# Kernel optimization log

Measured on AMD Instinct MI355X. Metric: run time of the kernel, lower is better.

Reference implementation:

```python
import jax, jax.numpy as jnp
import numpy as np

B, N, C, H = 16, 207, 64, 64

def setup_inputs() -> dict:
    key = jax.random.key(0)
    k1, k2, k3, k4, k5 = jax.random.split(key, 5)
    return {
        "x": jax.random.normal(k1, (B, N, C), dtype=jnp.float32),
        "state": jax.random.normal(k2, (B, N, 1, H), dtype=jnp.float32),
        "Wx": jax.random.normal(k3, (B, N, C, 3 * H), dtype=jnp.float32) * 0.1,
        "Wh": jax.random.normal(k4, (B, N, H, 3 * H), dtype=jnp.float32) * 0.1,
        "b": jax.random.normal(k5, (B, N, 1, 3 * H), dtype=jnp.float32) * 0.1,
    }

def reference(x, state, Wx, Wh, b):
    # x: [B,N,C] -> [B,N,1,C]; state (h): [B,N,1,H]
    if x.ndim == 3:
        x = x[..., None, :]
    h = state
    dim_hidden = Wh.shape[-2]
    # One fused batched matmul for x @ Wx, then split into r/z/c parts.
    xW = jnp.matmul(x, Wx)  # [B,N,1,3H]
    xr, xz, xc = jnp.split(xW, 3, axis=-1)
    Wrh, Wzh, Wch = jnp.split(Wh, 3, axis=-1)
    br, bz, bc = jnp.split(b, 3, axis=-1)
    r = jax.nn.sigmoid(xr + jnp.matmul(h, Wrh) + br)
    z = jax.nn.sigmoid(xz + jnp.matmul(h, Wzh) + bz)
    # Note torch precedence: r * h @ Wch == (r * h) @ Wch
    hc = jnp.tanh(xc + jnp.matmul(r * h, Wch) + bc)
    h_new = (1.0 - z) * h + z * hc  # [B,N,1,H]
    return h_new
```

## Files before the change

### kernel.cpp

```cpp
#include <hip/hip_runtime.h>
#include <math.h>


#define GC 64
#define GH 64
#define J3 192
#define WPP (GC * J3)

__global__ __launch_bounds__(192) void gru_cell_v2(
    const float* __restrict__ x,
    const float* __restrict__ state,
    const float* __restrict__ Wx,
    const float* __restrict__ Wh,
    const float* __restrict__ b,
    float* __restrict__ out)
{
    const int pos = blockIdx.x;
    const int t = threadIdx.x;
    const int jg = t % 48;
    const int rp = t / 48;

    __shared__ float x_s[GC];
    __shared__ float h_s[GH];
    __shared__ float wch_s[GC * GH];
    __shared__ float part[4][J3 + 4];
    __shared__ float rh_s[GH];
    __shared__ float z_s[GH];

    if (t < GC)           x_s[t]      = x[(size_t)pos * GC + t];
    else if (t < GC + GH) h_s[t - GC] = state[(size_t)pos * GH + (t - GC)];
    __syncthreads();

    const float4* __restrict__ Wx4 = (const float4*)(Wx + (size_t)pos * WPP);
    const float4* __restrict__ Wh4 = (const float4*)(Wh + (size_t)pos * WPP);

    float4 acc = {0.f, 0.f, 0.f, 0.f};
    const bool gate = (jg < 32);
    const int wchcol = 4 * (jg - 32);

    #pragma unroll 4
    for (int i = 0; i < 16; ++i) {
        const int c = 4 * i + rp;
        float4 wx4 = Wx4[i * J3 + t];
        float4 wh4 = Wh4[i * J3 + t];
        const float xs = x_s[c];
        acc.x += xs * wx4.x; acc.y += xs * wx4.y;
        acc.z += xs * wx4.z; acc.w += xs * wx4.w;
        if (gate) {
            const float hs = h_s[c];
            acc.x += hs * wh4.x; acc.y += hs * wh4.y;
            acc.z += hs * wh4.z; acc.w += hs * wh4.w;
        } else {
            *((float4*)&wch_s[c * GH + wchcol]) = wh4;
        }
    }

    *((float4*)&part[rp][4 * jg]) = acc;
    __syncthreads();

    float v = part[0][t] + part[1][t] + part[2][t] + part[3][t]
            + b[(size_t)pos * J3 + t];
    const float tc = v;
    if (t < GH) {
        float r = 1.f / (1.f + expf(-v));
        rh_s[t] = r * h_s[t];
    } else if (t < 2 * GH) {
        z_s[t - GH] = 1.f / (1.f + expf(-v));
    }
    __syncthreads();

    if (t >= 2 * GH) {
        const int jc = t - 2 * GH;
        float s = 0.f;
        #pragma unroll 8
        for (int k = 0; k < GH; ++k) s += rh_s[k] * wch_s[k * GH + jc];
        const float hc = tanhf(tc + s);
        const float z = z_s[jc];
        out[(size_t)pos * GH + jc] = (1.f - z) * h_s[jc] + z * hc;
    }
}

extern "C" void kernel_launch(void* const* d_in, const int* in_sizes, int n_in,
                              void* d_out, int out_size, void* d_ws, size_t ws_size,
                              hipStream_t stream) {
    const float* x     = (const float*)d_in[0];
    const float* state = (const float*)d_in[1];
    const float* Wx    = (const float*)d_in[2];
    const float* Wh    = (const float*)d_in[3];
    const float* b     = (const float*)d_in[4];
    float* out = (float*)d_out;

    const int npos = in_sizes[0] / GC;

    gru_cell_v2<<<npos, 192, 0, stream>>>(x, state, Wx, Wh, b, out);
}
```

Measured before the change: 337.5 us.

## Split GRU cell into r-gate phase then z/candidate phase with 256 threads

Restructures the per-position kernel into two phases. The first computes only the r gate from the first 64 columns of Wx/Wh. The second computes the z gate and the candidate, folding r*h into the Wh matmul so Wch no longer needs to be staged in shared memory. Block size grows to 256 with a 16- or 8-way row split, shared memory use drops, and the launch bound asks for more resident blocks. The cost is extra syncthreads, and the second half of the weights is read only after the r gate is done, which serializes part of the memory streaming.

```diff
diff --git a/kernel.cpp b/kernel.cpp
--- a/kernel.cpp
+++ b/kernel.cpp
@@ -7,7 +7,7 @@
 #define J3 192
 #define WPP (GC * J3)
 
-__global__ __launch_bounds__(192) void gru_cell_v2(
+__global__ __launch_bounds__(256, 8) void gru_cell_v3(
     const float* __restrict__ x,
     const float* __restrict__ state,
     const float* __restrict__ Wx,
@@ -17,66 +17,84 @@
 {
     const int pos = blockIdx.x;
     const int t = threadIdx.x;
-    const int jg = t % 48;
-    const int rp = t / 48;
 
     __shared__ float x_s[GC];
-    __shared__ float h_s[GH];
-    __shared__ float wch_s[GC * GH];
-    __shared__ float part[4][J3 + 4];
-    __shared__ float rh_s[GH];
+    __shared__ float mult_s[2 * GH];
+    __shared__ float part[1024];
     __shared__ float z_s[GH];
 
-    if (t < GC)           x_s[t]      = x[(size_t)pos * GC + t];
-    else if (t < GC + GH) h_s[t - GC] = state[(size_t)pos * GH + (t - GC)];
+    if (t < GC)           x_s[t]          = x[(size_t)pos * GC + t];
+    else if (t < GC + GH) mult_s[t - GC]  = state[(size_t)pos * GH + (t - GC)];
     __syncthreads();
 
     const float4* __restrict__ Wx4 = (const float4*)(Wx + (size_t)pos * WPP);
     const float4* __restrict__ Wh4 = (const float4*)(Wh + (size_t)pos * WPP);
 
-    float4 acc = {0.f, 0.f, 0.f, 0.f};
-    const bool gate = (jg < 32);
-    const int wchcol = 4 * (jg - 32);
-
-    #pragma unroll 4
-    for (int i = 0; i < 16; ++i) {
-        const int c = 4 * i + rp;
-        float4 wx4 = Wx4[i * J3 + t];
-        float4 wh4 = Wh4[i * J3 + t];
-        const float xs = x_s[c];
-        acc.x += xs * wx4.x; acc.y += xs * wx4.y;
-        acc.z += xs * wx4.z; acc.w += xs * wx4.w;
-        if (gate) {
-            const float hs = h_s[c];
-            acc.x += hs * wh4.x; acc.y += hs * wh4.y;
-            acc.z += hs * wh4.z; acc.w += hs * wh4.w;
-        } else {
-            *((float4*)&wch_s[c * GH + wchcol]) = wh4;
+    {
+        const int jg = t & 15;
+        const int rp = t >> 4;
+        float4 acc = {0.f, 0.f, 0.f, 0.f};
+        #pragma unroll
+        for (int k = 0; k < 4; ++k) {
+            const int c = rp + 16 * k;
+            const float4 wx4 = Wx4[c * 48 + jg];
+            const float4 wh4 = Wh4[c * 48 + jg];
+            const float xs = x_s[c];
+            const float hs = mult_s[c];
+            acc.x += xs * wx4.x + hs * wh4.x;
+            acc.y += xs * wx4.y + hs * wh4.y;
+            acc.z += xs * wx4.z + hs * wh4.z;
+            acc.w += xs * wx4.w + hs * wh4.w;
         }
-    }
-
-    *((float4*)&part[rp][4 * jg]) = acc;
-    __syncthreads();
-
-    float v = part[0][t] + part[1][t] + part[2][t] + part[3][t]
-            + b[(size_t)pos * J3 + t];
-    const float tc = v;
-    if (t < GH) {
-        float r = 1.f / (1.f + expf(-v));
-        rh_s[t] = r * h_s[t];
-    } else if (t < 2 * GH) {
-        z_s[t - GH] = 1.f / (1.f + expf(-v));
+        *((float4*)&part[rp * 64 + 4 * jg]) = acc;
     }
     __syncthreads();
 
-    if (t >= 2 * GH) {
-        const int jc = t - 2 * GH;
-        float s = 0.f;
-        #pragma unroll 8
-        for (int k = 0; k < GH; ++k) s += rh_s[k] * wch_s[k * GH + jc];
-        const float hc = tanhf(tc + s);
-        const float z = z_s[jc];
-        out[(size_t)pos * GH + jc] = (1.f - z) * h_s[jc] + z * hc;
+    if (t < GH) {
+        float v = b[(size_t)pos * J3 + t];
+        #pragma unroll
+        for (int rp = 0; rp < 16; ++rp) v += part[rp * 64 + t];
+        const float r = 1.f / (1.f + expf(-v));
+        mult_s[GH + t] = r * mult_s[t];
+    }
+    __syncthreads();
+
+    float vc = 0.f;
+    {
+        const int jg = t & 31;
+        const int rp = t >> 5;
+        const int msel = (jg & 16) << 2;
+        float4 acc = {0.f, 0.f, 0.f, 0.f};
+        #pragma unroll 4
+        for (int k = 0; k < 8; ++k) {
+            const int c = rp + 8 * k;
+            const float4 wx4 = Wx4[c * 48 + 16 + jg];
+            const float4 wh4 = Wh4[c * 48 + 16 + jg];
+            const float xs = x_s[c];
+            const float ms = mult_s[msel + c];
+            acc.x += xs * wx4.x + ms * wh4.x;
+            acc.y += xs * wx4.y + ms * wh4.y;
+            acc.z += xs * wx4.z + ms * wh4.z;
+            acc.w += xs * wx4.w + ms * wh4.w;
+        }
+        *((float4*)&part[rp * 128 + 4 * jg]) = acc;
+    }
+    __syncthreads();
+
+    if (t < 2 * GH) {
+        float v = b[(size_t)pos * J3 + GH + t];
+        #pragma unroll
+        for (int rp = 0; rp < 8; ++rp) v += part[rp * 128 + t];
+        if (t < GH) z_s[t] = 1.f / (1.f + expf(-v));
+        else        vc = v;
+    }
+    __syncthreads();
+
+    if (t >= GH && t < 2 * GH) {
+        const int j = t - GH;
+        const float hc = tanhf(vc);
+        const float z = z_s[j];
+        out[(size_t)pos * GH + j] = (1.f - z) * mult_s[j] + z * hc;
     }
 }
 
@@ -92,5 +110,5 @@
 
     const int npos = in_sizes[0] / GC;
 
-    gru_cell_v2<<<npos, 192, 0, stream>>>(x, state, Wx, Wh, b, out);
+    gru_cell_v3<<<npos, 256, 0, stream>>>(x, state, Wx, Wh, b, out);
 }
```

Measured after the change: 340.1 us. About the same (+0.8%).

## Map one wavefront per position with shuffle-based reductions, no shared memory

Applied to the files above, without the earlier changes.

Each 64-lane wavefront now handles one position, and each block packs four positions. Lanes split the C dimension into four row groups and reduce across them with xor shuffles, replacing the shared-memory staging, the partial-sum array and all block barriers. The r*h vector is rebuilt with shuffles so the candidate-gate matmul streams Wh directly from global memory. The cost is a heavier shuffle load, and npos/4 truncates, so position counts not divisible by four would be missed (3312 divides evenly).

```diff
diff --git a/kernel.cpp b/kernel.cpp
--- a/kernel.cpp
+++ b/kernel.cpp
@@ -7,7 +7,11 @@
 #define J3 192
 #define WPP (GC * J3)
 
-__global__ __launch_bounds__(192) void gru_cell_v2(
+__device__ __forceinline__ float sigm(float v) {
+    return 1.f / (1.f + expf(-v));
+}
+
+__global__ __launch_bounds__(256, 4) void gru_cell_v5(
     const float* __restrict__ x,
     const float* __restrict__ state,
     const float* __restrict__ Wx,
@@ -15,68 +19,112 @@
     const float* __restrict__ b,
     float* __restrict__ out)
 {
-    const int pos = blockIdx.x;
-    const int t = threadIdx.x;
-    const int jg = t % 48;
-    const int rp = t / 48;
+    const int lane = threadIdx.x & 63;
+    const int wid  = threadIdx.x >> 6;
+    const int pos  = blockIdx.x * 4 + wid;
 
-    __shared__ float x_s[GC];
-    __shared__ float h_s[GH];
-    __shared__ float wch_s[GC * GH];
-    __shared__ float part[4][J3 + 4];
-    __shared__ float rh_s[GH];
-    __shared__ float z_s[GH];
+    const int rr = lane >> 4;
+    const int jg = lane & 15;
 
-    if (t < GC)           x_s[t]      = x[(size_t)pos * GC + t];
-    else if (t < GC + GH) h_s[t - GC] = state[(size_t)pos * GH + (t - GC)];
-    __syncthreads();
+    const float xv  = x[(size_t)pos * GC + lane];
+    const float hv  = state[(size_t)pos * GH + lane];
+    const float bv0 = b[(size_t)pos * J3 + lane];
+    const float bv1 = b[(size_t)pos * J3 + 64 + lane];
+    const float bv2 = b[(size_t)pos * J3 + 128 + lane];
 
     const float4* __restrict__ Wx4 = (const float4*)(Wx + (size_t)pos * WPP);
     const float4* __restrict__ Wh4 = (const float4*)(Wh + (size_t)pos * WPP);
 
-    float4 acc = {0.f, 0.f, 0.f, 0.f};
-    const bool gate = (jg < 32);
-    const int wchcol = 4 * (jg - 32);
+    float4 accR = {0.f,0.f,0.f,0.f};
+    float4 accZ = {0.f,0.f,0.f,0.f};
+    float4 accC = {0.f,0.f,0.f,0.f};
 
-    #pragma unroll 4
-    for (int i = 0; i < 16; ++i) {
-        const int c = 4 * i + rp;
-        float4 wx4 = Wx4[i * J3 + t];
-        float4 wh4 = Wh4[i * J3 + t];
-        const float xs = x_s[c];
-        acc.x += xs * wx4.x; acc.y += xs * wx4.y;
-        acc.z += xs * wx4.z; acc.w += xs * wx4.w;
-        if (gate) {
-            const float hs = h_s[c];
-            acc.x += hs * wh4.x; acc.y += hs * wh4.y;
-            acc.z += hs * wh4.z; acc.w += hs * wh4.w;
-        } else {
-            *((float4*)&wch_s[c * GH + wchcol]) = wh4;
-        }
+    #pragma unroll
+    for (int k = 0; k < 16; ++k) {
+        const int c = 4 * k + rr;
+        const int base = c * 48 + jg;
+        const float4 wx0 = Wx4[base];
+        const float4 wx1 = Wx4[base + 16];
+        const float4 wx2 = Wx4[base + 32];
+        const float4 wh0 = Wh4[base];
+        const float xs = __shfl(xv, c);
+        const float hs = __shfl(hv, c);
+        accR.x += xs * wx0.x + hs * wh0.x;
+        accR.y += xs * wx0.y + hs * wh0.y;
+        accR.z += xs * wx0.z + hs * wh0.z;
+        accR.w += xs * wx0.w + hs * wh0.w;
+        accZ.x += xs * wx1.x; accZ.y += xs * wx1.y;
+        accZ.z += xs * wx1.z; accZ.w += xs * wx1.w;
+        accC.x += xs * wx2.x; accC.y += xs * wx2.y;
+        accC.z += xs * wx2.z; accC.w += xs * wx2.w;
     }
 
-    *((float4*)&part[rp][4 * jg]) = acc;
-    __syncthreads();
+    accR.x += __shfl_xor(accR.x, 16); accR.x += __shfl_xor(accR.x, 32);
+    accR.y += __shfl_xor(accR.y, 16); accR.y += __shfl_xor(accR.y, 32);
+    accR.z += __shfl_xor(accR.z, 16); accR.z += __shfl_xor(accR.z, 32);
+    accR.w += __shfl_xor(accR.w, 16); accR.w += __shfl_xor(accR.w, 32);
 
-    float v = part[0][t] + part[1][t] + part[2][t] + part[3][t]
-            + b[(size_t)pos * J3 + t];
-    const float tc = v;
-    if (t < GH) {
-        float r = 1.f / (1.f + expf(-v));
-        rh_s[t] = r * h_s[t];
-    } else if (t < 2 * GH) {
-        z_s[t - GH] = 1.f / (1.f + expf(-v));
+    float4 rv;
+    rv.x = sigm(accR.x + __shfl(bv0, 4 * jg + 0));
+    rv.y = sigm(accR.y + __shfl(bv0, 4 * jg + 1));
+    rv.z = sigm(accR.z + __shfl(bv0, 4 * jg + 2));
+    rv.w = sigm(accR.w + __shfl(bv0, 4 * jg + 3));
+
+    {
+        const int sl = lane >> 2;
+        const float c0 = __shfl(rv.x, sl);
+        const float c1 = __shfl(rv.y, sl);
+        const float c2 = __shfl(rv.z, sl);
+        const float c3 = __shfl(rv.w, sl);
+        const int q = lane & 3;
+        const float rl = (q == 0) ? c0 : (q == 1) ? c1 : (q == 2) ? c2 : c3;
+        rv.x = rl * hv;
     }
-    __syncthreads();
+    const float rhv = rv.x;
 
-    if (t >= 2 * GH) {
-        const int jc = t - 2 * GH;
-        float s = 0.f;
-        #pragma unroll 8
-        for (int k = 0; k < GH; ++k) s += rh_s[k] * wch_s[k * GH + jc];
-        const float hc = tanhf(tc + s);
-        const float z = z_s[jc];
-        out[(size_t)pos * GH + jc] = (1.f - z) * h_s[jc] + z * hc;
+    #pragma unroll
+    for (int k = 0; k < 16; ++k) {
+        const int c = 4 * k + rr;
+        const int base = c * 48 + jg;
+        const float4 wh1 = Wh4[base + 16];
+        const float4 wh2 = Wh4[base + 32];
+        const float hs = __shfl(hv, c);
+        const float rs = __shfl(rhv, c);
+        accZ.x += hs * wh1.x + 0.f;  accZ.y += hs * wh1.y;
+        accZ.z += hs * wh1.z;        accZ.w += hs * wh1.w;
+        accC.x += rs * wh2.x;        accC.y += rs * wh2.y;
+        accC.z += rs * wh2.z;        accC.w += rs * wh2.w;
+    }
+
+    accZ.x += __shfl_xor(accZ.x, 16); accZ.x += __shfl_xor(accZ.x, 32);
+    accZ.y += __shfl_xor(accZ.y, 16); accZ.y += __shfl_xor(accZ.y, 32);
+    accZ.z += __shfl_xor(accZ.z, 16); accZ.z += __shfl_xor(accZ.z, 32);
+    accZ.w += __shfl_xor(accZ.w, 16); accZ.w += __shfl_xor(accZ.w, 32);
+    accC.x += __shfl_xor(accC.x, 16); accC.x += __shfl_xor(accC.x, 32);
+    accC.y += __shfl_xor(accC.y, 16); accC.y += __shfl_xor(accC.y, 32);
+    accC.z += __shfl_xor(accC.z, 16); accC.z += __shfl_xor(accC.z, 32);
+    accC.w += __shfl_xor(accC.w, 16); accC.w += __shfl_xor(accC.w, 32);
+
+    float4 zv, hcv, ov;
+    zv.x  = sigm(accZ.x + __shfl(bv1, 4 * jg + 0));
+    zv.y  = sigm(accZ.y + __shfl(bv1, 4 * jg + 1));
+    zv.z  = sigm(accZ.z + __shfl(bv1, 4 * jg + 2));
+    zv.w  = sigm(accZ.w + __shfl(bv1, 4 * jg + 3));
+    hcv.x = tanhf(accC.x + __shfl(bv2, 4 * jg + 0));
+    hcv.y = tanhf(accC.y + __shfl(bv2, 4 * jg + 1));
+    hcv.z = tanhf(accC.z + __shfl(bv2, 4 * jg + 2));
+    hcv.w = tanhf(accC.w + __shfl(bv2, 4 * jg + 3));
+    const float h0 = __shfl(hv, 4 * jg + 0);
+    const float h1 = __shfl(hv, 4 * jg + 1);
+    const float h2 = __shfl(hv, 4 * jg + 2);
+    const float h3 = __shfl(hv, 4 * jg + 3);
+    ov.x = (1.f - zv.x) * h0 + zv.x * hcv.x;
+    ov.y = (1.f - zv.y) * h1 + zv.y * hcv.y;
+    ov.z = (1.f - zv.z) * h2 + zv.z * hcv.z;
+    ov.w = (1.f - zv.w) * h3 + zv.w * hcv.w;
+
+    if (lane < 16) {
+        ((float4*)(out + (size_t)pos * GH))[jg] = ov;
     }
 }
 
@@ -91,6 +139,7 @@
     float* out = (float*)d_out;
 
     const int npos = in_sizes[0] / GC;
+    const int nblk = npos / 4;
 
-    gru_cell_v2<<<npos, 192, 0, stream>>>(x, state, Wx, Wh, b, out);
+    gru_cell_v5<<<nblk, 256, 0, stream>>>(x, state, Wx, Wh, b, out);
 }
```

New measurement: 368.9 us. 9.3% more time.
